# Kernel tuning notes

Measured on AMD Instinct MI355X. Metric: run time of the kernel, lower is better.

Reference implementation:

```python
import jax, jax.numpy as jnp
import numpy as np

PRED_LEN = 30
H_DIM = 128
EMB_DIM = 16
DATA_DIM = 2
BATCH = 65536


def setup_inputs() -> dict:
    key = jax.random.key(0)
    ks = jax.random.split(key, 12)
    s = lambda k, shape, scale=1.0: jax.random.normal(k, shape, dtype=jnp.float32) * scale
    return {
        "last_obs": s(ks[0], (BATCH, DATA_DIM)),
        "last_obs_rel": s(ks[1], (BATCH, DATA_DIM)),
        "h0": s(ks[2], (1, BATCH, H_DIM), 0.1),
        "c0": s(ks[3], (1, BATCH, H_DIM), 0.1),
        "W_sp": s(ks[4], (EMB_DIM, DATA_DIM), 0.5),
        "b_sp": s(ks[5], (EMB_DIM,), 0.1),
        "W_ih": s(ks[6], (4 * H_DIM, EMB_DIM), 0.1),
        "b_ih": s(ks[7], (4 * H_DIM,), 0.05),
        "W_hh": s(ks[8], (4 * H_DIM, H_DIM), 0.1),
        "b_hh": s(ks[9], (4 * H_DIM,), 0.05),
        "W_out": s(ks[10], (DATA_DIM, H_DIM), 0.1),
        "b_out": s(ks[11], (DATA_DIM,), 0.05),
    }


def reference(last_obs, last_obs_rel, h0, c0, W_sp, b_sp, W_ih, b_ih, W_hh, b_hh, W_out, b_out):
    # eval mode: dropout is identity. PyTorch LSTM gate order: i, f, g, o.
    h = h0[0]  # (b, H)
    c = c0[0]  # (b, H)
    x = jnp.tanh(last_obs_rel @ W_sp.T + b_sp)  # (b, E)

    def step(carry, _):
        h, c, x = carry
        gates = x @ W_ih.T + b_ih + h @ W_hh.T + b_hh  # (b, 4H)
        i, f, g, o = jnp.split(gates, 4, axis=-1)
        c_new = jax.nn.sigmoid(f) * c + jax.nn.sigmoid(i) * jnp.tanh(g)
        h_new = jax.nn.sigmoid(o) * jnp.tanh(c_new)
        rel_pos = h_new @ W_out.T + b_out  # (b, 2)
        x_new = jnp.tanh(rel_pos @ W_sp.T + b_sp)
        return (h_new, c_new, x_new), rel_pos

    _, traj = jax.lax.scan(step, (h, c, x), None, length=PRED_LEN)  # (T, b, 2)
    return jnp.transpose(traj, (1, 0, 2))  # (b, T, 2)
```

## Files before the change

kernel.cpp:

```cpp
#include <hip/hip_runtime.h>

#define TSTEPS 30
#define KP2 136

#define LOG2E     1.44269504f
#define TWO_LOG2E 2.88539008f

#define SWZ(row, e) ((e) ^ ((((row) >> 3) & 1) << 4))

typedef _Float16 half8 __attribute__((ext_vector_type(8)));
typedef _Float16 half4 __attribute__((ext_vector_type(4)));
typedef float f32x4 __attribute__((ext_vector_type(4)));

#if __has_builtin(__builtin_amdgcn_mfma_f32_16x16x16f16)
#define XK16 1
#else
#define XK16 0
#endif

__device__ __forceinline__ float fexp2(float x) { return __builtin_amdgcn_exp2f(x); }
__device__ __forceinline__ float frcp(float x)  { return __builtin_amdgcn_rcpf(x); }
__device__ __forceinline__ float fsig_pre(float x)  { return frcp(1.0f + fexp2(-x)); }
__device__ __forceinline__ float ftanh_pre(float x) { return 1.0f - 2.0f * frcp(1.0f + fexp2(x)); }

__global__ __launch_bounds__(512, 2)
void lstm30_kernel(const float* __restrict__ last_obs_rel,
                   const float* __restrict__ h0,
                   const float* __restrict__ c0,
                   const float* __restrict__ W_sp,
                   const float* __restrict__ b_sp,
                   const float* __restrict__ W_ih,
                   const float* __restrict__ b_ih,
                   const float* __restrict__ W_hh,
                   const float* __restrict__ b_hh,
                   const float* __restrict__ W_out,
                   const float* __restrict__ b_out,
                   float* __restrict__ out)
{
    __shared__ _Float16 hA[32][KP2];
    __shared__ _Float16 lA[32][KP2];
#if XK16
    __shared__ _Float16 xS[2][16][20];
#else
    __shared__ _Float16 xS[2][16][32];
#endif

    const int tid  = threadIdx.x;
    const int w    = tid >> 6;
    const int L    = tid & 63;
    const int quad = L >> 4;
    const int col  = L & 15;
    const int base = blockIdx.x << 5;

#if XK16
    half8 Wf[4][4];
    half4 Wf4[4];
#else
    half8 Wf[4][5];
#endif
    float bias[4];
    #pragma unroll
    for (int nt = 0; nt < 4; ++nt) {
        const int G = nt * 128 + w * 16 + col;
        const float gsc = (nt == 2) ? TWO_LOG2E : LOG2E;
        bias[nt] = (b_ih[G] + b_hh[G]) * gsc;
        #pragma unroll
        for (int kc = 0; kc < 4; ++kc) {
            const int k0 = kc * 32 + quad * 8;
            const float4 a = *(const float4*)&W_hh[G * 128 + k0];
            const float4 b = *(const float4*)&W_hh[G * 128 + k0 + 4];
            half8 hh;
            hh[0] = (_Float16)(a.x * gsc); hh[1] = (_Float16)(a.y * gsc);
            hh[2] = (_Float16)(a.z * gsc); hh[3] = (_Float16)(a.w * gsc);
            hh[4] = (_Float16)(b.x * gsc); hh[5] = (_Float16)(b.y * gsc);
            hh[6] = (_Float16)(b.z * gsc); hh[7] = (_Float16)(b.w * gsc);
            Wf[nt][kc] = hh;
        }
#if XK16
        {
            const float4 a = *(const float4*)&W_ih[G * 16 + quad * 4];
            half4 h4;
            h4[0] = (_Float16)(a.x * gsc); h4[1] = (_Float16)(a.y * gsc);
            h4[2] = (_Float16)(a.z * gsc); h4[3] = (_Float16)(a.w * gsc);
            Wf4[nt] = h4;
        }
#else
        {
            const int k0 = 128 + quad * 8;
            float v[8];
            if (k0 < 144) {
                const float4 a = *(const float4*)&W_ih[G * 16 + (k0 - 128)];
                const float4 b = *(const float4*)&W_ih[G * 16 + (k0 - 128) + 4];
                v[0]=a.x; v[1]=a.y; v[2]=a.z; v[3]=a.w;
                v[4]=b.x; v[5]=b.y; v[6]=b.z; v[7]=b.w;
            } else {
                #pragma unroll
                for (int jj = 0; jj < 8; ++jj) v[jj] = 0.0f;
            }
            half8 hh;
            #pragma unroll
            for (int jj = 0; jj < 8; ++jj) hh[jj] = (_Float16)(v[jj] * gsc);
            Wf[nt][4] = hh;
        }
#endif
    }

    const float ws0 = W_sp[col * 2 + 0];
    const float ws1 = W_sp[col * 2 + 1];
    const float bs  = b_sp[col];
    const float bo0 = b_out[0], bo1 = b_out[1];

    half8 Ef[4];
    float einit = 0.0f;
    if (w < 4) {
        const bool isM = (w < 2);
        #pragma unroll
        for (int kc = 0; kc < 4; ++kc) {
            const int k0 = kc * 32 + quad * 8;
            const float4 a0 = *(const float4*)&W_out[k0];
            const float4 a1 = *(const float4*)&W_out[k0 + 4];
            const float4 b0 = *(const float4*)&W_out[128 + k0];
            const float4 b1 = *(const float4*)&W_out[128 + k0 + 4];
            float r0[8] = {a0.x,a0.y,a0.z,a0.w,a1.x,a1.y,a1.z,a1.w};
            float r1[8] = {b0.x,b0.y,b0.z,b0.w,b1.x,b1.y,b1.z,b1.w};
            half8 he;
            #pragma unroll
            for (int jj = 0; jj < 8; ++jj)
                he[jj] = isM ? (_Float16)((ws0 * r0[jj] + ws1 * r1[jj]) * TWO_LOG2E)
                             : (_Float16)((col == 0) ? r0[jj] : (col == 1) ? r1[jj] : 0.0f);
            Ef[kc] = he;
        }
        einit = isM ? (ws0 * bo0 + ws1 * bo1 + bs) * TWO_LOG2E
                    : ((col == 0) ? bo0 : (col == 1) ? bo1 : 0.0f);
    }

    float c[2][4];
    #pragma unroll
    for (int tt = 0; tt < 2; ++tt)
        #pragma unroll
        for (int r = 0; r < 4; ++r)
            c[tt][r] = c0[(base + tt * 16 + quad * 4 + r) * 128 + w * 16 + col];

    for (int idx = tid; idx < 32 * 128; idx += 512) {
        const int r = idx >> 7, k = idx & 127;
        const float v = h0[base * 128 + idx];
        const _Float16 hi = (_Float16)v;
        hA[r][SWZ(r, k)] = hi;
        lA[r][SWZ(r, k)] = (_Float16)(v - (float)hi);
    }
    {
        const int rr = tid >> 4;
        const float p0 = last_obs_rel[(base + rr) * 2 + 0];
        const float p1 = last_obs_rel[(base + rr) * 2 + 1];
        xS[rr >> 4][rr & 15][tid & 15] = (_Float16)ftanh_pre(TWO_LOG2E * (ws0 * p0 + ws1 * p1 + bs));
    }
#if !XK16
    for (int flat = tid; flat < 2 * 16 * 16; flat += 512) {
        const int T = flat >> 8, row = (flat >> 4) & 15;
        xS[T][row][16 + (flat & 15)] = (_Float16)0.0f;
    }
#endif
    __syncthreads();

    const int j = w * 16 + col;
    f32x4 accA[4], accB[4];

    for (int k = 0; k < TSTEPS; ++k) {
        {
            half8 a[4];
            #pragma unroll
            for (int kc = 0; kc < 4; ++kc)
                a[kc] = *(const half8*)&hA[col][SWZ(col, kc * 32 + quad * 8)];

            if (k > 0) {
#if XK16
                const half4 xb = *(const half4*)&xS[1][col][quad * 4];
                #pragma unroll
                for (int nt = 0; nt < 4; ++nt)
                    accB[nt] = __builtin_amdgcn_mfma_f32_16x16x16f16(xb, Wf4[nt], accB[nt], 0, 0, 0);
#else
                const half8 xb = *(const half8*)&xS[1][col][quad * 8];
                #pragma unroll
                for (int nt = 0; nt < 4; ++nt)
                    accB[nt] = __builtin_amdgcn_mfma_f32_16x16x32_f16(xb, Wf[nt][4], accB[nt], 0, 0, 0);
#endif
            }

            #pragma unroll
            for (int nt = 0; nt < 4; ++nt) {
                f32x4 bv = {bias[nt], bias[nt], bias[nt], bias[nt]};
                accA[nt] = bv;
            }
            f32x4 eacc = {einit, einit, einit, einit};

            #pragma unroll
            for (int kc = 0; kc < 4; ++kc)
                #pragma unroll
                for (int nt = 0; nt < 4; ++nt)
                    accA[nt] = __builtin_amdgcn_mfma_f32_16x16x32_f16(a[kc], Wf[nt][kc], accA[nt], 0, 0, 0);

            if (k > 0) {
                #pragma unroll
                for (int r = 0; r < 2; ++r) {
                    const int row = 16 + quad * 4 + r;
                    const float gi = fsig_pre(accB[0][r]);
                    const float gf = fsig_pre(accB[1][r]);
                    const float gg = ftanh_pre(accB[2][r]);
                    const float go = fsig_pre(accB[3][r]);
                    c[1][r] = gf * c[1][r] + gi * gg;
                    const float h = go * ftanh_pre(TWO_LOG2E * c[1][r]);
                    const _Float16 hi = (_Float16)h;
                    hA[row][SWZ(row, j)] = hi;
                    lA[row][SWZ(row, j)] = (_Float16)(h - (float)hi);
                }
            }

            if (k > 0 && w == 0) {
                #pragma unroll
                for (int kc = 0; kc < 4; ++kc)
                    eacc = __builtin_amdgcn_mfma_f32_16x16x32_f16(a[kc], Ef[kc], eacc, 0, 0, 0);
            }
            if (k > 0 && w == 2) {
                #pragma unroll
                for (int kc = 0; kc < 4; ++kc)
                    eacc = __builtin_amdgcn_mfma_f32_16x16x32_f16(a[kc], Ef[kc], eacc, 0, 0, 0);
                half8 aL[4];
                #pragma unroll
                for (int kc = 0; kc < 4; ++kc)
                    aL[kc] = *(const half8*)&lA[col][SWZ(col, kc * 32 + quad * 8)];
                #pragma unroll
                for (int kc = 0; kc < 4; ++kc)
                    eacc = __builtin_amdgcn_mfma_f32_16x16x32_f16(aL[kc], Ef[kc], eacc, 0, 0, 0);
            }

            if (k > 0) {
                #pragma unroll
                for (int r = 2; r < 4; ++r) {
                    const int row = 16 + quad * 4 + r;
                    const float gi = fsig_pre(accB[0][r]);
                    const float gf = fsig_pre(accB[1][r]);
                    const float gg = ftanh_pre(accB[2][r]);
                    const float go = fsig_pre(accB[3][r]);
                    c[1][r] = gf * c[1][r] + gi * gg;
                    const float h = go * ftanh_pre(TWO_LOG2E * c[1][r]);
                    const _Float16 hi = (_Float16)h;
                    hA[row][SWZ(row, j)] = hi;
                    lA[row][SWZ(row, j)] = (_Float16)(h - (float)hi);
                }
            }

            if (k > 0 && w == 0) {
                #pragma unroll
                for (int r = 0; r < 4; ++r)
                    xS[0][quad * 4 + r][col] = (_Float16)ftanh_pre(eacc[r]);
            }
            if (k > 0 && w == 2 && col < 2) {
                #pragma unroll
                for (int r = 0; r < 4; ++r)
                    out[(base + quad * 4 + r) * (TSTEPS * 2) + (k - 1) * 2 + col] = eacc[r];
            }
            __syncthreads();
        }
        {
            half8 a[4];
            #pragma unroll
            for (int kc = 0; kc < 4; ++kc)
                a[kc] = *(const half8*)&hA[16 + col][SWZ(16 + col, kc * 32 + quad * 8)];

            {
#if XK16
                const half4 xa = *(const half4*)&xS[0][col][quad * 4];
                #pragma unroll
                for (int nt = 0; nt < 4; ++nt)
                    accA[nt] = __builtin_amdgcn_mfma_f32_16x16x16f16(xa, Wf4[nt], accA[nt], 0, 0, 0);
#else
                const half8 xa = *(const half8*)&xS[0][col][quad * 8];
                #pragma unroll
                for (int nt = 0; nt < 4; ++nt)
                    accA[nt] = __builtin_amdgcn_mfma_f32_16x16x32_f16(xa, Wf[nt][4], accA[nt], 0, 0, 0);
#endif
            }

            #pragma unroll
            for (int nt = 0; nt < 4; ++nt) {
                f32x4 bv = {bias[nt], bias[nt], bias[nt], bias[nt]};
                accB[nt] = bv;
            }
            f32x4 eacc = {einit, einit, einit, einit};

            #pragma unroll
            for (int kc = 0; kc < 4; ++kc)
                #pragma unroll
                for (int nt = 0; nt < 4; ++nt)
                    accB[nt] = __builtin_amdgcn_mfma_f32_16x16x32_f16(a[kc], Wf[nt][kc], accB[nt], 0, 0, 0);

            {
                #pragma unroll
                for (int r = 0; r < 2; ++r) {
                    const int row = quad * 4 + r;
                    const float gi = fsig_pre(accA[0][r]);
                    const float gf = fsig_pre(accA[1][r]);
                    const float gg = ftanh_pre(accA[2][r]);
                    const float go = fsig_pre(accA[3][r]);
                    c[0][r] = gf * c[0][r] + gi * gg;
                    const float h = go * ftanh_pre(TWO_LOG2E * c[0][r]);
                    const _Float16 hi = (_Float16)h;
                    hA[row][SWZ(row, j)] = hi;
                    lA[row][SWZ(row, j)] = (_Float16)(h - (float)hi);
                }
            }

            if (w == 1) {
                #pragma unroll
                for (int kc = 0; kc < 4; ++kc)
                    eacc = __builtin_amdgcn_mfma_f32_16x16x32_f16(a[kc], Ef[kc], eacc, 0, 0, 0);
            }
            if (w == 3) {
                #pragma unroll
                for (int kc = 0; kc < 4; ++kc)
                    eacc = __builtin_amdgcn_mfma_f32_16x16x32_f16(a[kc], Ef[kc], eacc, 0, 0, 0);
                half8 aL[4];
                #pragma unroll
                for (int kc = 0; kc < 4; ++kc)
                    aL[kc] = *(const half8*)&lA[16 + col][SWZ(16 + col, kc * 32 + quad * 8)];
                #pragma unroll
                for (int kc = 0; kc < 4; ++kc)
                    eacc = __builtin_amdgcn_mfma_f32_16x16x32_f16(aL[kc], Ef[kc], eacc, 0, 0, 0);
            }

            {
                #pragma unroll
                for (int r = 2; r < 4; ++r) {
                    const int row = quad * 4 + r;
                    const float gi = fsig_pre(accA[0][r]);
                    const float gf = fsig_pre(accA[1][r]);
                    const float gg = ftanh_pre(accA[2][r]);
                    const float go = fsig_pre(accA[3][r]);
                    c[0][r] = gf * c[0][r] + gi * gg;
                    const float h = go * ftanh_pre(TWO_LOG2E * c[0][r]);
                    const _Float16 hi = (_Float16)h;
                    hA[row][SWZ(row, j)] = hi;
                    lA[row][SWZ(row, j)] = (_Float16)(h - (float)hi);
                }
            }

            if (k > 0 && w == 1) {
                #pragma unroll
                for (int r = 0; r < 4; ++r)
                    xS[1][quad * 4 + r][col] = (_Float16)ftanh_pre(eacc[r]);
            }
            if (k > 0 && w == 3 && col < 2) {
                #pragma unroll
                for (int r = 0; r < 4; ++r)
                    out[(base + 16 + quad * 4 + r) * (TSTEPS * 2) + (k - 1) * 2 + col] = eacc[r];
            }
            __syncthreads();
        }
    }

    {
        {
#if XK16
            const half4 xb = *(const half4*)&xS[1][col][quad * 4];
            #pragma unroll
            for (int nt = 0; nt < 4; ++nt)
                accB[nt] = __builtin_amdgcn_mfma_f32_16x16x16f16(xb, Wf4[nt], accB[nt], 0, 0, 0);
#else
            const half8 xb = *(const half8*)&xS[1][col][quad * 8];
            #pragma unroll
            for (int nt = 0; nt < 4; ++nt)
                accB[nt] = __builtin_amdgcn_mfma_f32_16x16x32_f16(xb, Wf[nt][4], accB[nt], 0, 0, 0);
#endif
        }
        if (w == 2) {
            f32x4 eacc = {einit, einit, einit, einit};
            #pragma unroll
            for (int kc = 0; kc < 4; ++kc) {
                const half8 aH = *(const half8*)&hA[col][SWZ(col, kc * 32 + quad * 8)];
                eacc = __builtin_amdgcn_mfma_f32_16x16x32_f16(aH, Ef[kc], eacc, 0, 0, 0);
            }
            #pragma unroll
            for (int kc = 0; kc < 4; ++kc) {
                const half8 aL = *(const half8*)&lA[col][SWZ(col, kc * 32 + quad * 8)];
                eacc = __builtin_amdgcn_mfma_f32_16x16x32_f16(aL, Ef[kc], eacc, 0, 0, 0);
            }
            if (col < 2) {
                #pragma unroll
                for (int r = 0; r < 4; ++r)
                    out[(base + quad * 4 + r) * (TSTEPS * 2) + (TSTEPS - 1) * 2 + col] = eacc[r];
            }
        }
        #pragma unroll
        for (int r = 0; r < 4; ++r) {
            const int row = 16 + quad * 4 + r;
            const float gi = fsig_pre(accB[0][r]);
            const float gf = fsig_pre(accB[1][r]);
            const float gg = ftanh_pre(accB[2][r]);
            const float go = fsig_pre(accB[3][r]);
            c[1][r] = gf * c[1][r] + gi * gg;
            const float h = go * ftanh_pre(TWO_LOG2E * c[1][r]);
            const _Float16 hi = (_Float16)h;
            hA[row][SWZ(row, j)] = hi;
            lA[row][SWZ(row, j)] = (_Float16)(h - (float)hi);
        }
        __syncthreads();
        if (w == 3) {
            f32x4 eacc = {einit, einit, einit, einit};
            #pragma unroll
            for (int kc = 0; kc < 4; ++kc) {
                const half8 aH = *(const half8*)&hA[16 + col][SWZ(16 + col, kc * 32 + quad * 8)];
                eacc = __builtin_amdgcn_mfma_f32_16x16x32_f16(aH, Ef[kc], eacc, 0, 0, 0);
            }
            #pragma unroll
            for (int kc = 0; kc < 4; ++kc) {
                const half8 aL = *(const half8*)&lA[16 + col][SWZ(16 + col, kc * 32 + quad * 8)];
                eacc = __builtin_amdgcn_mfma_f32_16x16x32_f16(aL, Ef[kc], eacc, 0, 0, 0);
            }
            if (col < 2) {
                #pragma unroll
                for (int r = 0; r < 4; ++r)
                    out[(base + 16 + quad * 4 + r) * (TSTEPS * 2) + (TSTEPS - 1) * 2 + col] = eacc[r];
            }
        }
    }
}

extern "C" void kernel_launch(void* const* d_in, const int* in_sizes, int n_in,
                              void* d_out, int out_size, void* d_ws, size_t ws_size,
                              hipStream_t stream) {
    const float* last_obs_rel = (const float*)d_in[1];
    const float* h0    = (const float*)d_in[2];
    const float* c0    = (const float*)d_in[3];
    const float* W_sp  = (const float*)d_in[4];
    const float* b_sp  = (const float*)d_in[5];
    const float* W_ih  = (const float*)d_in[6];
    const float* b_ih  = (const float*)d_in[7];
    const float* W_hh  = (const float*)d_in[8];
    const float* b_hh  = (const float*)d_in[9];
    const float* W_out = (const float*)d_in[10];
    const float* b_out = (const float*)d_in[11];
    float* out = (float*)d_out;

    const int batch = in_sizes[2] / 128;
    lstm30_kernel<<<dim3(batch / 32), dim3(512), 0, stream>>>(
        last_obs_rel, h0, c0, W_sp, b_sp, W_ih, b_ih, W_hh, b_hh, W_out, b_out, out);
}
```

Measured before the change: 627.1 us.

## Move output-projection fragments to shared memory and raise occupancy target

The per-wave Ef MFMA B-fragments (16 halves of registers per lane) are moved into a shared-memory table built once by waves 0 and 2, and every use now reads them from LDS. Launch bounds go from 2 to 4 blocks per CU, so the compiler must fit the kernel in far fewer VGPRs. The goal is more resident blocks to hide the latency of the serial recurrence. The cost is extra LDS reads each timestep and a likely risk of register spills under the tighter register budget, which could hurt.

After: 1.841 ms. 194% more time.

```diff
diff --git a/kernel.cpp b/kernel.cpp
--- a/kernel.cpp
+++ b/kernel.cpp
@@ -23,7 +23,7 @@
 __device__ __forceinline__ float fsig_pre(float x)  { return frcp(1.0f + fexp2(-x)); }
 __device__ __forceinline__ float ftanh_pre(float x) { return 1.0f - 2.0f * frcp(1.0f + fexp2(x)); }
 
-__global__ __launch_bounds__(512, 2)
+__global__ __launch_bounds__(512, 4)
 void lstm30_kernel(const float* __restrict__ last_obs_rel,
                    const float* __restrict__ h0,
                    const float* __restrict__ c0,
@@ -44,6 +44,7 @@
 #else
     __shared__ _Float16 xS[2][16][32];
 #endif
+    __shared__ __align__(16) _Float16 efS[2][64][40];
 
     const int tid  = threadIdx.x;
     const int w    = tid >> 6;
@@ -110,28 +111,29 @@
     const float bs  = b_sp[col];
     const float bo0 = b_out[0], bo1 = b_out[1];
 
-    half8 Ef[4];
-    float einit = 0.0f;
-    if (w < 4) {
+    float einit;
+    {
         const bool isM = (w < 2);
-        #pragma unroll
-        for (int kc = 0; kc < 4; ++kc) {
-            const int k0 = kc * 32 + quad * 8;
-            const float4 a0 = *(const float4*)&W_out[k0];
-            const float4 a1 = *(const float4*)&W_out[k0 + 4];
-            const float4 b0 = *(const float4*)&W_out[128 + k0];
-            const float4 b1 = *(const float4*)&W_out[128 + k0 + 4];
-            float r0[8] = {a0.x,a0.y,a0.z,a0.w,a1.x,a1.y,a1.z,a1.w};
-            float r1[8] = {b0.x,b0.y,b0.z,b0.w,b1.x,b1.y,b1.z,b1.w};
-            half8 he;
-            #pragma unroll
-            for (int jj = 0; jj < 8; ++jj)
-                he[jj] = isM ? (_Float16)((ws0 * r0[jj] + ws1 * r1[jj]) * TWO_LOG2E)
-                             : (_Float16)((col == 0) ? r0[jj] : (col == 1) ? r1[jj] : 0.0f);
-            Ef[kc] = he;
-        }
         einit = isM ? (ws0 * bo0 + ws1 * bo1 + bs) * TWO_LOG2E
                     : ((col == 0) ? bo0 : (col == 1) ? bo1 : 0.0f);
+        if (w == 0 || w == 2) {
+            #pragma unroll
+            for (int kc = 0; kc < 4; ++kc) {
+                const int k0 = kc * 32 + quad * 8;
+                const float4 a0 = *(const float4*)&W_out[k0];
+                const float4 a1 = *(const float4*)&W_out[k0 + 4];
+                const float4 b0 = *(const float4*)&W_out[128 + k0];
+                const float4 b1 = *(const float4*)&W_out[128 + k0 + 4];
+                float r0[8] = {a0.x,a0.y,a0.z,a0.w,a1.x,a1.y,a1.z,a1.w};
+                float r1[8] = {b0.x,b0.y,b0.z,b0.w,b1.x,b1.y,b1.z,b1.w};
+                half8 he;
+                #pragma unroll
+                for (int jj = 0; jj < 8; ++jj)
+                    he[jj] = isM ? (_Float16)((ws0 * r0[jj] + ws1 * r1[jj]) * TWO_LOG2E)
+                                 : (_Float16)((col == 0) ? r0[jj] : (col == 1) ? r1[jj] : 0.0f);
+                *(half8*)&efS[w >> 1][L][kc * 8] = he;
+            }
+        }
     }
 
     float c[2][4];
@@ -217,20 +219,23 @@
 
             if (k > 0 && w == 0) {
                 #pragma unroll
-                for (int kc = 0; kc < 4; ++kc)
-                    eacc = __builtin_amdgcn_mfma_f32_16x16x32_f16(a[kc], Ef[kc], eacc, 0, 0, 0);
+                for (int kc = 0; kc < 4; ++kc) {
+                    const half8 ef = *(const half8*)&efS[0][L][kc * 8];
+                    eacc = __builtin_amdgcn_mfma_f32_16x16x32_f16(a[kc], ef, eacc, 0, 0, 0);
+                }
             }
             if (k > 0 && w == 2) {
                 #pragma unroll
-                for (int kc = 0; kc < 4; ++kc)
-                    eacc = __builtin_amdgcn_mfma_f32_16x16x32_f16(a[kc], Ef[kc], eacc, 0, 0, 0);
-                half8 aL[4];
-                #pragma unroll
-                for (int kc = 0; kc < 4; ++kc)
-                    aL[kc] = *(const half8*)&lA[col][SWZ(col, kc * 32 + quad * 8)];
-                #pragma unroll
-                for (int kc = 0; kc < 4; ++kc)
-                    eacc = __builtin_amdgcn_mfma_f32_16x16x32_f16(aL[kc], Ef[kc], eacc, 0, 0, 0);
+                for (int kc = 0; kc < 4; ++kc) {
+                    const half8 ef = *(const half8*)&efS[1][L][kc * 8];
+                    eacc = __builtin_amdgcn_mfma_f32_16x16x32_f16(a[kc], ef, eacc, 0, 0, 0);
+                }
+                #pragma unroll
+                for (int kc = 0; kc < 4; ++kc) {
+                    const half8 aL = *(const half8*)&lA[col][SWZ(col, kc * 32 + quad * 8)];
+                    const half8 ef = *(const half8*)&efS[1][L][kc * 8];
+                    eacc = __builtin_amdgcn_mfma_f32_16x16x32_f16(aL, ef, eacc, 0, 0, 0);
+                }
             }
 
             if (k > 0) {
@@ -312,20 +317,23 @@
 
             if (w == 1) {
                 #pragma unroll
-                for (int kc = 0; kc < 4; ++kc)
-                    eacc = __builtin_amdgcn_mfma_f32_16x16x32_f16(a[kc], Ef[kc], eacc, 0, 0, 0);
+                for (int kc = 0; kc < 4; ++kc) {
+                    const half8 ef = *(const half8*)&efS[0][L][kc * 8];
+                    eacc = __builtin_amdgcn_mfma_f32_16x16x32_f16(a[kc], ef, eacc, 0, 0, 0);
+                }
             }
             if (w == 3) {
                 #pragma unroll
-                for (int kc = 0; kc < 4; ++kc)
-                    eacc = __builtin_amdgcn_mfma_f32_16x16x32_f16(a[kc], Ef[kc], eacc, 0, 0, 0);
-                half8 aL[4];
-                #pragma unroll
-                for (int kc = 0; kc < 4; ++kc)
-                    aL[kc] = *(const half8*)&lA[16 + col][SWZ(16 + col, kc * 32 + quad * 8)];
-                #pragma unroll
-                for (int kc = 0; kc < 4; ++kc)
-                    eacc = __builtin_amdgcn_mfma_f32_16x16x32_f16(aL[kc], Ef[kc], eacc, 0, 0, 0);
+                for (int kc = 0; kc < 4; ++kc) {
+                    const half8 ef = *(const half8*)&efS[1][L][kc * 8];
+                    eacc = __builtin_amdgcn_mfma_f32_16x16x32_f16(a[kc], ef, eacc, 0, 0, 0);
+                }
+                #pragma unroll
+                for (int kc = 0; kc < 4; ++kc) {
+                    const half8 aL = *(const half8*)&lA[16 + col][SWZ(16 + col, kc * 32 + quad * 8)];
+                    const half8 ef = *(const half8*)&efS[1][L][kc * 8];
+                    eacc = __builtin_amdgcn_mfma_f32_16x16x32_f16(aL, ef, eacc, 0, 0, 0);
+                }
             }
 
             {
@@ -377,12 +385,14 @@
             #pragma unroll
             for (int kc = 0; kc < 4; ++kc) {
                 const half8 aH = *(const half8*)&hA[col][SWZ(col, kc * 32 + quad * 8)];
-                eacc = __builtin_amdgcn_mfma_f32_16x16x32_f16(aH, Ef[kc], eacc, 0, 0, 0);
+                const half8 ef = *(const half8*)&efS[1][L][kc * 8];
+                eacc = __builtin_amdgcn_mfma_f32_16x16x32_f16(aH, ef, eacc, 0, 0, 0);
             }
             #pragma unroll
             for (int kc = 0; kc < 4; ++kc) {
                 const half8 aL = *(const half8*)&lA[col][SWZ(col, kc * 32 + quad * 8)];
-                eacc = __builtin_amdgcn_mfma_f32_16x16x32_f16(aL, Ef[kc], eacc, 0, 0, 0);
+                const half8 ef = *(const half8*)&efS[1][L][kc * 8];
+                eacc = __builtin_amdgcn_mfma_f32_16x16x32_f16(aL, ef, eacc, 0, 0, 0);
             }
             if (col < 2) {
                 #pragma unroll
@@ -409,12 +419,14 @@
             #pragma unroll
             for (int kc = 0; kc < 4; ++kc) {
                 const half8 aH = *(const half8*)&hA[16 + col][SWZ(16 + col, kc * 32 + quad * 8)];
-                eacc = __builtin_amdgcn_mfma_f32_16x16x32_f16(aH, Ef[kc], eacc, 0, 0, 0);
+                const half8 ef = *(const half8*)&efS[1][L][kc * 8];
+                eacc = __builtin_amdgcn_mfma_f32_16x16x32_f16(aH, ef, eacc, 0, 0, 0);
             }
             #pragma unroll
             for (int kc = 0; kc < 4; ++kc) {
                 const half8 aL = *(const half8*)&lA[16 + col][SWZ(16 + col, kc * 32 + quad * 8)];
-                eacc = __builtin_amdgcn_mfma_f32_16x16x32_f16(aL, Ef[kc], eacc, 0, 0, 0);
+                const half8 ef = *(const half8*)&efS[1][L][kc * 8];
+                eacc = __builtin_amdgcn_mfma_f32_16x16x32_f16(aL, ef, eacc, 0, 0, 0);
             }
             if (col < 2) {
                 #pragma unroll
```

## Process 64 batch rows per block as two interleaved 32-row pipelines

Applied to the files above, without the earlier changes.

Doubles the rows handled per workgroup from 32 to 64 by running two independent two-tile LSTM pipelines side by side. Each wave reuses its register-resident W_hh fragments across twice as many MFMAs per barrier, and all eight waves now share the output and embedding projection work. This halves the number of blocks, amortises weight loads, and gives the scheduler more independent MFMA chains to hide latency. The cost is higher register pressure (two more accumulator sets and c state) under launch_bounds(512,2), more LDS use, and half the grid size.

After: 592.3 us. -5.5%, faster.

```diff
diff --git a/kernel.cpp b/kernel.cpp
--- a/kernel.cpp
+++ b/kernel.cpp
@@ -22,6 +22,19 @@
 __device__ __forceinline__ float frcp(float x)  { return __builtin_amdgcn_rcpf(x); }
 __device__ __forceinline__ float fsig_pre(float x)  { return frcp(1.0f + fexp2(-x)); }
 __device__ __forceinline__ float ftanh_pre(float x) { return 1.0f - 2.0f * frcp(1.0f + fexp2(x)); }
+
+#define CELL_ROW(ACC, CC, ROW, R) do {                                  \
+    const float gi_ = fsig_pre(ACC[0][R]);                              \
+    const float gf_ = fsig_pre(ACC[1][R]);                              \
+    const float gg_ = ftanh_pre(ACC[2][R]);                             \
+    const float go_ = fsig_pre(ACC[3][R]);                              \
+    CC = gf_ * CC + gi_ * gg_;                                          \
+    const float hv_ = go_ * ftanh_pre(TWO_LOG2E * CC);                  \
+    const _Float16 hh_ = (_Float16)hv_;                                 \
+    const int row_ = (ROW);                                             \
+    hS[row_][SWZ(row_, j)] = hh_;                                       \
+    lS[row_][SWZ(row_, j)] = (_Float16)(hv_ - (float)hh_);              \
+} while (0)
 
 __global__ __launch_bounds__(512, 2)
 void lstm30_kernel(const float* __restrict__ last_obs_rel,
@@ -37,12 +50,12 @@
                    const float* __restrict__ b_out,
                    float* __restrict__ out)
 {
-    __shared__ _Float16 hA[32][KP2];
-    __shared__ _Float16 lA[32][KP2];
+    __shared__ _Float16 hS[64][KP2];
+    __shared__ _Float16 lS[64][KP2];
 #if XK16
-    __shared__ _Float16 xS[2][16][20];
-#else
-    __shared__ _Float16 xS[2][16][32];
+    __shared__ _Float16 xS[4][16][20];
+#else
+    __shared__ _Float16 xS[4][16][32];
 #endif
 
     const int tid  = threadIdx.x;
@@ -50,7 +63,7 @@
     const int L    = tid & 63;
     const int quad = L >> 4;
     const int col  = L & 15;
-    const int base = blockIdx.x << 5;
+    const int base = blockIdx.x << 6;
 
 #if XK16
     half8 Wf[4][4];
@@ -111,9 +124,9 @@
     const float bo0 = b_out[0], bo1 = b_out[1];
 
     half8 Ef[4];
-    float einit = 0.0f;
-    if (w < 4) {
-        const bool isM = (w < 2);
+    float einit;
+    {
+        const bool isM = ((w & 2) == 0);
         #pragma unroll
         for (int kc = 0; kc < 4; ++kc) {
             const int k0 = kc * 32 + quad * 8;
@@ -134,118 +147,126 @@
                     : ((col == 0) ? bo0 : (col == 1) ? bo1 : 0.0f);
     }
 
-    float c[2][4];
+    float c[4][4];
     #pragma unroll
-    for (int tt = 0; tt < 2; ++tt)
+    for (int t = 0; t < 4; ++t)
         #pragma unroll
         for (int r = 0; r < 4; ++r)
-            c[tt][r] = c0[(base + tt * 16 + quad * 4 + r) * 128 + w * 16 + col];
-
-    for (int idx = tid; idx < 32 * 128; idx += 512) {
-        const int r = idx >> 7, k = idx & 127;
+            c[t][r] = c0[(base + t * 16 + quad * 4 + r) * 128 + w * 16 + col];
+
+    for (int idx = tid; idx < 64 * 128; idx += 512) {
+        const int r = idx >> 7, kk = idx & 127;
         const float v = h0[base * 128 + idx];
         const _Float16 hi = (_Float16)v;
-        hA[r][SWZ(r, k)] = hi;
-        lA[r][SWZ(r, k)] = (_Float16)(v - (float)hi);
-    }
-    {
-        const int rr = tid >> 4;
+        hS[r][SWZ(r, kk)] = hi;
+        lS[r][SWZ(r, kk)] = (_Float16)(v - (float)hi);
+    }
+    #pragma unroll
+    for (int hlf = 0; hlf < 2; ++hlf) {
+        const int rr = (tid >> 4) + hlf * 32;
         const float p0 = last_obs_rel[(base + rr) * 2 + 0];
         const float p1 = last_obs_rel[(base + rr) * 2 + 1];
         xS[rr >> 4][rr & 15][tid & 15] = (_Float16)ftanh_pre(TWO_LOG2E * (ws0 * p0 + ws1 * p1 + bs));
     }
 #if !XK16
-    for (int flat = tid; flat < 2 * 16 * 16; flat += 512) {
-        const int T = flat >> 8, row = (flat >> 4) & 15;
-        xS[T][row][16 + (flat & 15)] = (_Float16)0.0f;
+    for (int flat = tid; flat < 4 * 16 * 16; flat += 512) {
+        xS[flat >> 8][(flat >> 4) & 15][16 + (flat & 15)] = (_Float16)0.0f;
     }
 #endif
     __syncthreads();
 
     const int j = w * 16 + col;
-    f32x4 accA[4], accB[4];
+    f32x4 accT0[4], accT1[4], accT2[4], accT3[4];
 
     for (int k = 0; k < TSTEPS; ++k) {
         {
-            half8 a[4];
-            #pragma unroll
-            for (int kc = 0; kc < 4; ++kc)
-                a[kc] = *(const half8*)&hA[col][SWZ(col, kc * 32 + quad * 8)];
+            half8 a0[4], a2[4];
+            #pragma unroll
+            for (int kc = 0; kc < 4; ++kc) {
+                a0[kc] = *(const half8*)&hS[col][SWZ(col, kc * 32 + quad * 8)];
+                a2[kc] = *(const half8*)&hS[32 + col][SWZ(32 + col, kc * 32 + quad * 8)];
+            }
 
             if (k > 0) {
 #if XK16
-                const half4 xb = *(const half4*)&xS[1][col][quad * 4];
-                #pragma unroll
-                for (int nt = 0; nt < 4; ++nt)
-                    accB[nt] = __builtin_amdgcn_mfma_f32_16x16x16f16(xb, Wf4[nt], accB[nt], 0, 0, 0);
-#else
-                const half8 xb = *(const half8*)&xS[1][col][quad * 8];
-                #pragma unroll
-                for (int nt = 0; nt < 4; ++nt)
-                    accB[nt] = __builtin_amdgcn_mfma_f32_16x16x32_f16(xb, Wf[nt][4], accB[nt], 0, 0, 0);
+                const half4 x1 = *(const half4*)&xS[1][col][quad * 4];
+                const half4 x3 = *(const half4*)&xS[3][col][quad * 4];
+                #pragma unroll
+                for (int nt = 0; nt < 4; ++nt) {
+                    accT1[nt] = __builtin_amdgcn_mfma_f32_16x16x16f16(x1, Wf4[nt], accT1[nt], 0, 0, 0);
+                    accT3[nt] = __builtin_amdgcn_mfma_f32_16x16x16f16(x3, Wf4[nt], accT3[nt], 0, 0, 0);
+                }
+#else
+                const half8 x1 = *(const half8*)&xS[1][col][quad * 8];
+                const half8 x3 = *(const half8*)&xS[3][col][quad * 8];
+                #pragma unroll
+                for (int nt = 0; nt < 4; ++nt) {
+                    accT1[nt] = __builtin_amdgcn_mfma_f32_16x16x32_f16(x1, Wf[nt][4], accT1[nt], 0, 0, 0);
+                    accT3[nt] = __builtin_amdgcn_mfma_f32_16x16x32_f16(x3, Wf[nt][4], accT3[nt], 0, 0, 0);
+                }
 #endif
             }
 
             #pragma unroll
             for (int nt = 0; nt < 4; ++nt) {
                 f32x4 bv = {bias[nt], bias[nt], bias[nt], bias[nt]};
-                accA[nt] = bv;
+                accT0[nt] = bv;
+                accT2[nt] = bv;
             }
             f32x4 eacc = {einit, einit, einit, einit};
 
             #pragma unroll
             for (int kc = 0; kc < 4; ++kc)
                 #pragma unroll
-                for (int nt = 0; nt < 4; ++nt)
-                    accA[nt] = __builtin_amdgcn_mfma_f32_16x16x32_f16(a[kc], Wf[nt][kc], accA[nt], 0, 0, 0);
+                for (int nt = 0; nt < 4; ++nt) {
+                    accT0[nt] = __builtin_amdgcn_mfma_f32_16x16x32_f16(a0[kc], Wf[nt][kc], accT0[nt], 0, 0, 0);
+                    accT2[nt] = __builtin_amdgcn_mfma_f32_16x16x32_f16(a2[kc], Wf[nt][kc], accT2[nt], 0, 0, 0);
+                }
 
             if (k > 0) {
                 #pragma unroll
                 for (int r = 0; r < 2; ++r) {
-                    const int row = 16 + quad * 4 + r;
-                    const float gi = fsig_pre(accB[0][r]);
-                    const float gf = fsig_pre(accB[1][r]);
-                    const float gg = ftanh_pre(accB[2][r]);
-                    const float go = fsig_pre(accB[3][r]);
-                    c[1][r] = gf * c[1][r] + gi * gg;
-                    const float h = go * ftanh_pre(TWO_LOG2E * c[1][r]);
-                    const _Float16 hi = (_Float16)h;
-                    hA[row][SWZ(row, j)] = hi;
-                    lA[row][SWZ(row, j)] = (_Float16)(h - (float)hi);
+                    CELL_ROW(accT1, c[1][r], 16 + quad * 4 + r, r);
+                    CELL_ROW(accT3, c[3][r], 48 + quad * 4 + r, r);
                 }
             }
 
             if (k > 0 && w == 0) {
                 #pragma unroll
                 for (int kc = 0; kc < 4; ++kc)
-                    eacc = __builtin_amdgcn_mfma_f32_16x16x32_f16(a[kc], Ef[kc], eacc, 0, 0, 0);
+                    eacc = __builtin_amdgcn_mfma_f32_16x16x32_f16(a0[kc], Ef[kc], eacc, 0, 0, 0);
+            }
+            if (k > 0 && w == 1) {
+                #pragma unroll
+                for (int kc = 0; kc < 4; ++kc)
+                    eacc = __builtin_amdgcn_mfma_f32_16x16x32_f16(a2[kc], Ef[kc], eacc, 0, 0, 0);
             }
             if (k > 0 && w == 2) {
                 #pragma unroll
                 for (int kc = 0; kc < 4; ++kc)
-                    eacc = __builtin_amdgcn_mfma_f32_16x16x32_f16(a[kc], Ef[kc], eacc, 0, 0, 0);
-                half8 aL[4];
-                #pragma unroll
-                for (int kc = 0; kc < 4; ++kc)
-                    aL[kc] = *(const half8*)&lA[col][SWZ(col, kc * 32 + quad * 8)];
-                #pragma unroll
-                for (int kc = 0; kc < 4; ++kc)
-                    eacc = __builtin_amdgcn_mfma_f32_16x16x32_f16(aL[kc], Ef[kc], eacc, 0, 0, 0);
+                    eacc = __builtin_amdgcn_mfma_f32_16x16x32_f16(a0[kc], Ef[kc], eacc, 0, 0, 0);
+                #pragma unroll
+                for (int kc = 0; kc < 4; ++kc) {
+                    const half8 aL = *(const half8*)&lS[col][SWZ(col, kc * 32 + quad * 8)];
+                    eacc = __builtin_amdgcn_mfma_f32_16x16x32_f16(aL, Ef[kc], eacc, 0, 0, 0);
+                }
+            }
+            if (k > 0 && w == 3) {
+                #pragma unroll
+                for (int kc = 0; kc < 4; ++kc)
+                    eacc = __builtin_amdgcn_mfma_f32_16x16x32_f16(a2[kc], Ef[kc], eacc, 0, 0, 0);
+                #pragma unroll
+                for (int kc = 0; kc < 4; ++kc) {
+                    const half8 aL = *(const half8*)&lS[32 + col][SWZ(32 + col, kc * 32 + quad * 8)];
+                    eacc = __builtin_amdgcn_mfma_f32_16x16x32_f16(aL, Ef[kc], eacc, 0, 0, 0);
+                }
             }
 
             if (k > 0) {
                 #pragma unroll
                 for (int r = 2; r < 4; ++r) {
-                    const int row = 16 + quad * 4 + r;
-                    const float gi = fsig_pre(accB[0][r]);
-                    const float gf = fsig_pre(accB[1][r]);
-                    const float gg = ftanh_pre(accB[2][r]);
-                    const float go = fsig_pre(accB[3][r]);
-                    c[1][r] = gf * c[1][r] + gi * gg;
-                    const float h = go * ftanh_pre(TWO_LOG2E * c[1][r]);
-                    const _Float16 hi = (_Float16)h;
-                    hA[row][SWZ(row, j)] = hi;
-                    lA[row][SWZ(row, j)] = (_Float16)(h - (float)hi);
+                    CELL_ROW(accT1, c[1][r], 16 + quad * 4 + r, r);
+                    CELL_ROW(accT3, c[3][r], 48 + quad * 4 + r, r);
                 }
             }
 
@@ -254,105 +275,133 @@
                 for (int r = 0; r < 4; ++r)
                     xS[0][quad * 4 + r][col] = (_Float16)ftanh_pre(eacc[r]);
             }
+            if (k > 0 && w == 1) {
+                #pragma unroll
+                for (int r = 0; r < 4; ++r)
+                    xS[2][quad * 4 + r][col] = (_Float16)ftanh_pre(eacc[r]);
+            }
             if (k > 0 && w == 2 && col < 2) {
                 #pragma unroll
                 for (int r = 0; r < 4; ++r)
                     out[(base + quad * 4 + r) * (TSTEPS * 2) + (k - 1) * 2 + col] = eacc[r];
             }
+            if (k > 0 && w == 3 && col < 2) {
+                #pragma unroll
+                for (int r = 0; r < 4; ++r)
+                    out[(base + 32 + quad * 4 + r) * (TSTEPS * 2) + (k - 1) * 2 + col] = eacc[r];
+            }
             __syncthreads();
         }
         {
-            half8 a[4];
-            #pragma unroll
-            for (int kc = 0; kc < 4; ++kc)
-                a[kc] = *(const half8*)&hA[16 + col][SWZ(16 + col, kc * 32 + quad * 8)];
+            half8 a1[4], a3[4];
+            #pragma unroll
+            for (int kc = 0; kc < 4; ++kc) {
+                a1[kc] = *(const half8*)&hS[16 + col][SWZ(16 + col, kc * 32 + quad * 8)];
+                a3[kc] = *(const half8*)&hS[48 + col][SWZ(48 + col, kc * 32 + quad * 8)];
+            }
 
             {
 #if XK16
-                const half4 xa = *(const half4*)&xS[0][col][quad * 4];
-                #pragma unroll
-                for (int nt = 0; nt < 4; ++nt)
-                    accA[nt] = __builtin_amdgcn_mfma_f32_16x16x16f16(xa, Wf4[nt], accA[nt], 0, 0, 0);
-#else
-                const half8 xa = *(const half8*)&xS[0][col][quad * 8];
-                #pragma unroll
-                for (int nt = 0; nt < 4; ++nt)
-                    accA[nt] = __builtin_amdgcn_mfma_f32_16x16x32_f16(xa, Wf[nt][4], accA[nt], 0, 0, 0);
+                const half4 x0 = *(const half4*)&xS[0][col][quad * 4];
+                const half4 x2 = *(const half4*)&xS[2][col][quad * 4];
+                #pragma unroll
+                for (int nt = 0; nt < 4; ++nt) {
+                    accT0[nt] = __builtin_amdgcn_mfma_f32_16x16x16f16(x0, Wf4[nt], accT0[nt], 0, 0, 0);
+                    accT2[nt] = __builtin_amdgcn_mfma_f32_16x16x16f16(x2, Wf4[nt], accT2[nt], 0, 0, 0);
+                }
+#else
+                const half8 x0 = *(const half8*)&xS[0][col][quad * 8];
+                const half8 x2 = *(const half8*)&xS[2][col][quad * 8];
+                #pragma unroll
+                for (int nt = 0; nt < 4; ++nt) {
+                    accT0[nt] = __builtin_amdgcn_mfma_f32_16x16x32_f16(x0, Wf[nt][4], accT0[nt], 0, 0, 0);
+                    accT2[nt] = __builtin_amdgcn_mfma_f32_16x16x32_f16(x2, Wf[nt][4], accT2[nt], 0, 0, 0);
+                }
 #endif
             }
 
             #pragma unroll
             for (int nt = 0; nt < 4; ++nt) {
                 f32x4 bv = {bias[nt], bias[nt], bias[nt], bias[nt]};
-                accB[nt] = bv;
+                accT1[nt] = bv;
+                accT3[nt] = bv;
             }
             f32x4 eacc = {einit, einit, einit, einit};
 
             #pragma unroll
             for (int kc = 0; kc < 4; ++kc)
                 #pragma unroll
-                for (int nt = 0; nt < 4; ++nt)
-                    accB[nt] = __builtin_amdgcn_mfma_f32_16x16x32_f16(a[kc], Wf[nt][kc], accB[nt], 0, 0, 0);
+                for (int nt = 0; nt < 4; ++nt) {
+                    accT1[nt] = __builtin_amdgcn_mfma_f32_16x16x32_f16(a1[kc], Wf[nt][kc], accT1[nt], 0, 0, 0);
+                    accT3[nt] = __builtin_amdgcn_mfma_f32_16x16x32_f16(a3[kc], Wf[nt][kc], accT3[nt], 0, 0, 0);
+                }
 
             {
                 #pragma unroll
                 for (int r = 0; r < 2; ++r) {
-                    const int row = quad * 4 + r;
-                    const float gi = fsig_pre(accA[0][r]);
-                    const float gf = fsig_pre(accA[1][r]);
-                    const float gg = ftanh_pre(accA[2][r]);
-                    const float go = fsig_pre(accA[3][r]);
-                    c[0][r] = gf * c[0][r] + gi * gg;
-                    const float h = go * ftanh_pre(TWO_LOG2E * c[0][r]);
-                    const _Float16 hi = (_Float16)h;
-                    hA[row][SWZ(row, j)] = hi;
-                    lA[row][SWZ(row, j)] = (_Float16)(h - (float)hi);
-                }
-            }
-
-            if (w == 1) {
-                #pragma unroll
-                for (int kc = 0; kc < 4; ++kc)
-                    eacc = __builtin_amdgcn_mfma_f32_16x16x32_f16(a[kc], Ef[kc], eacc, 0, 0, 0);
-            }
-            if (w == 3) {
-                #pragma unroll
-                for (int kc = 0; kc < 4; ++kc)
-                    eacc = __builtin_amdgcn_mfma_f32_16x16x32_f16(a[kc], Ef[kc], eacc, 0, 0, 0);
-                half8 aL[4];
-                #pragma unroll
-                for (int kc = 0; kc < 4; ++kc)
-                    aL[kc] = *(const half8*)&lA[16 + col][SWZ(16 + col, kc * 32 + quad * 8)];
-                #pragma unroll
-                for (int kc = 0; kc < 4; ++kc)
-                    eacc = __builtin_amdgcn_mfma_f32_16x16x32_f16(aL[kc], Ef[kc], eacc, 0, 0, 0);
+                    CELL_ROW(accT0, c[0][r], quad * 4 + r, r);
+                    CELL_ROW(accT2, c[2][r], 32 + quad * 4 + r, r);
+                }
+            }
+
+            if (w == 4) {
+                #pragma unroll
+                for (int kc = 0; kc < 4; ++kc)
+                    eacc = __builtin_amdgcn_mfma_f32_16x16x32_f16(a1[kc], Ef[kc], eacc, 0, 0, 0);
+            }
+            if (w == 5) {
+                #pragma unroll
+                for (int kc = 0; kc < 4; ++kc)
+                    eacc = __builtin_amdgcn_mfma_f32_16x16x32_f16(a3[kc], Ef[kc], eacc, 0, 0, 0);
+            }
+            if (w == 6) {
+                #pragma unroll
+                for (int kc = 0; kc < 4; ++kc)
+                    eacc = __builtin_amdgcn_mfma_f32_16x16x32_f16(a1[kc], Ef[kc], eacc, 0, 0, 0);
+                #pragma unroll
+                for (int kc = 0; kc < 4; ++kc) {
+                    const half8 aL = *(const half8*)&lS[16 + col][SWZ(16 + col, kc * 32 + quad * 8)];
+                    eacc = __builtin_amdgcn_mfma_f32_16x16x32_f16(aL, Ef[kc], eacc, 0, 0, 0);
+                }
+            }
+            if (w == 7) {
+                #pragma unroll
+                for (int kc = 0; kc < 4; ++kc)
+                    eacc = __builtin_amdgcn_mfma_f32_16x16x32_f16(a3[kc], Ef[kc], eacc, 0, 0, 0);
+                #pragma unroll
+                for (int kc = 0; kc < 4; ++kc) {
+                    const half8 aL = *(const half8*)&lS[48 + col][SWZ(48 + col, kc * 32 + quad * 8)];
+                    eacc = __builtin_amdgcn_mfma_f32_16x16x32_f16(aL, Ef[kc], eacc, 0, 0, 0);
+                }
             }
 
             {
                 #pragma unroll
                 for (int r = 2; r < 4; ++r) {
-                    const int row = quad * 4 + r;
-                    const float gi = fsig_pre(accA[0][r]);
-                    const float gf = fsig_pre(accA[1][r]);
-                    const float gg = ftanh_pre(accA[2][r]);
-                    const float go = fsig_pre(accA[3][r]);
-                    c[0][r] = gf * c[0][r] + gi * gg;
-                    const float h = go * ftanh_pre(TWO_LOG2E * c[0][r]);
-                    const _Float16 hi = (_Float16)h;
-                    hA[row][SWZ(row, j)] = hi;
-                    lA[row][SWZ(row, j)] = (_Float16)(h - (float)hi);
-                }
-            }
-
-            if (k > 0 && w == 1) {
+                    CELL_ROW(accT0, c[0][r], quad * 4 + r, r);
+                    CELL_ROW(accT2, c[2][r], 32 + quad * 4 + r, r);
+                }
+            }
+
+            if (k > 0 && w == 4) {
                 #pragma unroll
                 for (int r = 0; r < 4; ++r)
                     xS[1][quad * 4 + r][col] = (_Float16)ftanh_pre(eacc[r]);
             }
-            if (k > 0 && w == 3 && col < 2) {
+            if (k > 0 && w == 5) {
+                #pragma unroll
+                for (int r = 0; r < 4; ++r)
+                    xS[3][quad * 4 + r][col] = (_Float16)ftanh_pre(eacc[r]);
+            }
+            if (k > 0 && w == 6 && col < 2) {
                 #pragma unroll
                 for (int r = 0; r < 4; ++r)
                     out[(base + 16 + quad * 4 + r) * (TSTEPS * 2) + (k - 1) * 2 + col] = eacc[r];
+            }
+            if (k > 0 && w == 7 && col < 2) {
+                #pragma unroll
+                for (int r = 0; r < 4; ++r)
+                    out[(base + 48 + quad * 4 + r) * (TSTEPS * 2) + (k - 1) * 2 + col] = eacc[r];
             }
             __syncthreads();
         }
@@ -361,65 +410,99 @@
     {
         {
 #if XK16
-            const half4 xb = *(const half4*)&xS[1][col][quad * 4];
-            #pragma unroll
-            for (int nt = 0; nt < 4; ++nt)
-                accB[nt] = __builtin_amdgcn_mfma_f32_16x16x16f16(xb, Wf4[nt], accB[nt], 0, 0, 0);
-#else
-            const half8 xb = *(const half8*)&xS[1][col][quad * 8];
-            #pragma unroll
-            for (int nt = 0; nt < 4; ++nt)
-                accB[nt] = __builtin_amdgcn_mfma_f32_16x16x32_f16(xb, Wf[nt][4], accB[nt], 0, 0, 0);
+            const half4 x1 = *(const half4*)&xS[1][col][quad * 4];
+            const half4 x3 = *(const half4*)&xS[3][col][quad * 4];
+            #pragma unroll
+            for (int nt = 0; nt < 4; ++nt) {
+                accT1[nt] = __builtin_amdgcn_mfma_f32_16x16x16f16(x1, Wf4[nt], accT1[nt], 0, 0, 0);
+                accT3[nt] = __builtin_amdgcn_mfma_f32_16x16x16f16(x3, Wf4[nt], accT3[nt], 0, 0, 0);
+            }
+#else
+            const half8 x1 = *(const half8*)&xS[1][col][quad * 8];
+            const half8 x3 = *(const half8*)&xS[3][col][quad * 8];
+            #pragma unroll
+            for (int nt = 0; nt < 4; ++nt) {
+                accT1[nt] = __builtin_amdgcn_mfma_f32_16x16x32_f16(x1, Wf[nt][4], accT1[nt], 0, 0, 0);
+                accT3[nt] = __builtin_amdgcn_mfma_f32_16x16x32_f16(x3, Wf[nt][4], accT3[nt], 0, 0, 0);
+            }
 #endif
         }
         if (w == 2) {
             f32x4 eacc = {einit, einit, einit, einit};
             #pragma unroll
             for (int kc = 0; kc < 4; ++kc) {
-                const half8 aH = *(const half8*)&hA[col][SWZ(col, kc * 32 + quad * 8)];
+                const half8 aH = *(const half8*)&hS[col][SWZ(col, kc * 32 + quad * 8)];
                 eacc = __builtin_amdgcn_mfma_f32_16x16x32_f16(aH, Ef[kc], eacc, 0, 0, 0);
             }
             #pragma unroll
             for (int kc = 0; kc < 4; ++kc) {
-                const half8 aL = *(const half8*)&lA[col][SWZ(col, kc * 32 + quad * 8)];
+                const half8 aL = *(const half8*)&lS[col][SWZ(col, kc * 32 + quad * 8)];
                 eacc = __builtin_amdgcn_mfma_f32_16x16x32_f16(aL, Ef[kc], eacc, 0, 0, 0);
             }
             if (col < 2) {
                 #pragma unroll
                 for (int r = 0; r < 4; ++r)
                     out[(base + quad * 4 + r) * (TSTEPS * 2) + (TSTEPS - 1) * 2 + col] = eacc[r];
+            }
+        }
+        if (w == 3) {
+            f32x4 eacc = {einit, einit, einit, einit};
+            #pragma unroll
+            for (int kc = 0; kc < 4; ++kc) {
+                const half8 aH = *(const half8*)&hS[32 + col][SWZ(32 + col, kc * 32 + quad * 8)];
+                eacc = __builtin_amdgcn_mfma_f32_16x16x32_f16(aH, Ef[kc], eacc, 0, 0, 0);
+            }
+            #pragma unroll
+            for (int kc = 0; kc < 4; ++kc) {
+                const half8 aL = *(const half8*)&lS[32 + col][SWZ(32 + col, kc * 32 + quad * 8)];
+                eacc = __builtin_amdgcn_mfma_f32_16x16x32_f16(aL, Ef[kc], eacc, 0, 0, 0);
+            }
+            if (col < 2) {
+                #pragma unroll
+                for (int r = 0; r < 4; ++r)
+                    out[(base + 32 + quad * 4 + r) * (TSTEPS * 2) + (TSTEPS - 1) * 2 + col] = eacc[r];
             }
         }
         #pragma unroll
         for (int r = 0; r < 4; ++r) {
-            const int row = 16 + quad * 4 + r;
-            const float gi = fsig_pre(accB[0][r]);
-            const float gf = fsig_pre(accB[1][r]);
-            const float gg = ftanh_pre(accB[2][r]);
-            const float go = fsig_pre(accB[3][r]);
-            c[1][r] = gf * c[1][r] + gi * gg;
-            const float h = go * ftanh_pre(TWO_LOG2E * c[1][r]);
-            const _Float16 hi = (_Float16)h;
-            hA[row][SWZ(row, j)] = hi;
-            lA[row][SWZ(row, j)] = (_Float16)(h - (float)hi);
+            CELL_ROW(accT1, c[1][r], 16 + quad * 4 + r, r);
+            CELL_ROW(accT3, c[3][r], 48 + quad * 4 + r, r);
         }
         __syncthreads();
-        if (w == 3) {
+        if (w == 6) {
             f32x4 eacc = {einit, einit, einit, einit};
             #pragma unroll
             for (int kc = 0; kc < 4; ++kc) {
-                const half8 aH = *(const half8*)&hA[16 + col][SWZ(16 + col, kc * 32 + quad * 8)];
+                const half8 aH = *(const half8*)&hS[16 + col][SWZ(16 + col, kc * 32 + quad * 8)];
                 eacc = __builtin_amdgcn_mfma_f32_16x16x32_f16(aH, Ef[kc], eacc, 0, 0, 0);
             }
             #pragma unroll
             for (int kc = 0; kc < 4; ++kc) {
-                const half8 aL = *(const half8*)&lA[16 + col][SWZ(16 + col, kc * 32 + quad * 8)];
+                const half8 aL = *(const half8*)&lS[16 + col][SWZ(16 + col, kc * 32 + quad * 8)];
                 eacc = __builtin_amdgcn_mfma_f32_16x16x32_f16(aL, Ef[kc], eacc, 0, 0, 0);
             }
             if (col < 2) {
                 #pragma unroll
                 for (int r = 0; r < 4; ++r)
                     out[(base + 16 + quad * 4 + r) * (TSTEPS * 2) + (TSTEPS - 1) * 2 + col] = eacc[r];
+            }
+        }
+        if (w == 7) {
+            f32x4 eacc = {einit, einit, einit, einit};
+            #pragma unroll
+            for (int kc = 0; kc < 4; ++kc) {
+                const half8 aH = *(const half8*)&hS[48 + col][SWZ(48 + col, kc * 32 + quad * 8)];
+                eacc = __builtin_amdgcn_mfma_f32_16x16x32_f16(aH, Ef[kc], eacc, 0, 0, 0);
+            }
+            #pragma unroll
+            for (int kc = 0; kc < 4; ++kc) {
+                const half8 aL = *(const half8*)&lS[48 + col][SWZ(48 + col, kc * 32 + quad * 8)];
+                eacc = __builtin_amdgcn_mfma_f32_16x16x32_f16(aL, Ef[kc], eacc, 0, 0, 0);
+            }
+            if (col < 2) {
+                #pragma unroll
+                for (int r = 0; r < 4; ++r)
+                    out[(base + 48 + quad * 4 + r) * (TSTEPS * 2) + (TSTEPS - 1) * 2 + col] = eacc[r];
             }
         }
     }
@@ -442,6 +525,6 @@
     float* out = (float*)d_out;
 
     const int batch = in_sizes[2] / 128;
-    lstm30_kernel<<<dim3(batch / 32), dim3(512), 0, stream>>>(
+    lstm30_kernel<<<dim3(batch / 64), dim3(512), 0, stream>>>(
         last_obs_rel, h0, c0, W_sp, b_sp, W_ih, b_ih, W_hh, b_hh, W_out, b_out, out);
 }
```
